# Optimization experiments

Hardware: AMD Instinct MI355X
Metric: run time of the kernel (lower is better)

The kernel has to match this reference:

```python
import jax, jax.numpy as jnp
import numpy as np

N = 1_048_576   # nodes
E = 8_388_608   # edges
G = 32_768      # graphs
D = 9           # node embedding dim (hardcoded emb_dim=9 in source)
H = 2 * D       # GIN MLP hidden
L = 3           # num_layers
ATOM_V, BOND_V = 119, 6
BN_EPS = 1e-5


def setup_inputs() -> dict:
    key = jax.random.key(0)
    ks = jax.random.split(key, 12)
    f = lambda i, shape: jax.random.normal(ks[i], shape, jnp.float32) * 0.1
    return {
        'atom_emb': f(0, (9, ATOM_V, D)),
        'bond_emb': f(1, (L, 3, BOND_V, D)),
        'eps_gin': jnp.zeros((L,), jnp.float32),
        'W1': f(2, (L, D, H)), 'b1': jnp.zeros((L, H)),
        'bn1_g': jnp.ones((L, H)), 'bn1_b': jnp.zeros((L, H)),
        'W2': f(3, (L, H, D)), 'b2': jnp.zeros((L, D)),
        'bno_g': jnp.ones((L, D)), 'bno_b': jnp.zeros((L, D)),
        'vnW1': f(4, (L - 1, D, H)), 'vnb1': jnp.zeros((L - 1, H)),
        'vnbn1_g': jnp.ones((L - 1, H)), 'vnbn1_b': jnp.zeros((L - 1, H)),
        'vnW2': f(5, (L - 1, H, D)), 'vnb2': jnp.zeros((L - 1, D)),
        'vnbn2_g': jnp.ones((L - 1, D)), 'vnbn2_b': jnp.zeros((L - 1, D)),
        'x': jax.random.randint(ks[6], (N, 9), 0, 2),
        'edge_index': jax.random.randint(ks[7], (2, E), 0, N),
        'edge_attr': jax.random.randint(ks[8], (E, 3), 0, 2),
        'batch': jnp.sort(jax.random.randint(ks[9], (N,), 0, G)),
        'num_graphs': G,
    }


def _bn(h, g, b):
    # BatchNorm1d in training mode: batch mean / biased variance
    m = h.mean(axis=0)
    v = h.var(axis=0)
    return (h - m) * jax.lax.rsqrt(v + BN_EPS) * g + b


def reference(atom_emb, bond_emb, eps_gin, W1, b1, bn1_g, bn1_b, W2, b2,
              bno_g, bno_b, vnW1, vnb1, vnbn1_g, vnbn1_b, vnW2, vnb2,
              vnbn2_g, vnbn2_b, x, edge_index, edge_attr, batch, num_graphs):
    n_nodes = x.shape[0]
    src, dst = edge_index[0], edge_index[1]
    # AtomEncoder: sum of per-field embeddings -> [N, D]
    h = atom_emb[jnp.arange(atom_emb.shape[0])[None, :], x].sum(axis=1)
    vn = jnp.zeros((num_graphs, h.shape[1]), h.dtype)  # virtualnode emb init 0
    num_layers = W1.shape[0]
    for l in range(num_layers):
        h_in = h + vn[batch]                              # broadcast VN to nodes
        # BondEncoder for this layer -> [E, D]
        e = bond_emb[l][jnp.arange(3)[None, :], edge_attr].sum(axis=1)
        # GIN message: relu(x_j + e), sum-aggregate at target
        msg = jax.nn.relu(h_in[src] + e)
        aggr = jax.ops.segment_sum(msg, dst, num_segments=n_nodes)
        z = (1.0 + eps_gin[l]) * h_in + aggr
        z = jax.nn.relu(_bn(z @ W1[l] + b1[l], bn1_g[l], bn1_b[l])) @ W2[l] + b2[l]
        z = _bn(z, bno_g[l], bno_b[l])
        if l < num_layers - 1:
            z = jax.nn.relu(z)
        h_new = z + h_in                                   # residual=True
        if l < num_layers - 1:
            vn_tmp = jax.ops.segment_sum(h_in, batch, num_segments=num_graphs) + vn
            t = jax.nn.relu(_bn(vn_tmp @ vnW1[l] + vnb1[l], vnbn1_g[l], vnbn1_b[l]))
            t = jax.nn.relu(_bn(t @ vnW2[l] + vnb2[l], vnbn2_g[l], vnbn2_b[l]))
            vn = vn + t                                    # VN residual
        h = h_new
    pooled = jax.ops.segment_sum(h, batch, num_segments=num_graphs)  # global_add_pool
    return jnp.sum(pooled, axis=0, keepdims=True)          # [1, D]
```

## Files before the change

kernel.cpp:

```cpp
#include <hip/hip_runtime.h>
#include <hip/hip_fp8.h>

#define NN 1048576
#define NE 8388608
#define NG 32768
#define DD 9
#define HH 18
#define BN_EPS 1e-5f

#define NPB 512
#define NB  2048
#define NGRP 64
#define P1B 512
#define P3MAX 5120
#define P3KEYS 2048

#define NSUM1 0
#define NSQ1  18
#define NSUM2 36
#define NSQ2  45
#define OUTS  54
#define VBASE 4096
#define VSUM1 (VBASE+0)
#define VSQ1  (VBASE+18)
#define VSUM2 (VBASE+36)
#define VSQ2  (VBASE+45)
#define STATS_FLOATS 4224

typedef float fv4 __attribute__((ext_vector_type(4)));
typedef unsigned uv4 __attribute__((ext_vector_type(4)));

__device__ __forceinline__ float waveReduce(float v) {
#pragma unroll
  for (int off = 32; off > 0; off >>= 1) v += __shfl_down(v, off, 64);
  return v;
}
__device__ __forceinline__ unsigned f8enc(float f) {
  __hip_fp8_e4m3 v(f);
  return (unsigned)v.__x;
}
__device__ __forceinline__ float f8dec(unsigned b) {
  __hip_fp8_e4m3 v;
  v.__x = (__hip_fp8_storage_t)b;
  return (float)v;
}
__device__ __forceinline__ unsigned bf16r(float x) {
  unsigned u = __float_as_uint(x);
  unsigned r = u + 0x7FFFu + ((u >> 16) & 1u);
  return r >> 16;
}
__device__ __forceinline__ unsigned pk2(float a, float b) {
  return bf16r(a) | (bf16r(b) << 16);
}
__device__ __forceinline__ float lo16(unsigned u) { return __uint_as_float(u << 16); }
__device__ __forceinline__ float hi16(unsigned u) { return __uint_as_float(u & 0xFFFF0000u); }

__device__ __forceinline__ void pack9(uv4* __restrict__ b8, unsigned short* __restrict__ b1,
                                      size_t n, const float* v) {
  uv4 p;
  p.x = pk2(v[0], v[1]); p.y = pk2(v[2], v[3]);
  p.z = pk2(v[4], v[5]); p.w = pk2(v[6], v[7]);
  __builtin_nontemporal_store(p, &b8[n]);
  __builtin_nontemporal_store((unsigned short)bf16r(v[8]), &b1[n]);
}
__device__ __forceinline__ void unpack9(const uv4* __restrict__ b8,
                                        const unsigned short* __restrict__ b1,
                                        size_t n, float* v) {
  uv4 P = __builtin_nontemporal_load(&b8[n]);
  unsigned short s = b1[n];
  v[0] = lo16(P.x); v[1] = hi16(P.x); v[2] = lo16(P.y); v[3] = hi16(P.y);
  v[4] = lo16(P.z); v[5] = hi16(P.z); v[6] = lo16(P.w); v[7] = hi16(P.w);
  v[8] = __uint_as_float((unsigned)s << 16);
}


__global__ void __launch_bounds__(1024)
k_counthist(const int* __restrict__ ei, int* __restrict__ cnt_pad,
            int* __restrict__ blkcnt) {
  __shared__ int hist[NB];
  int tid = threadIdx.x;
  for (int i = tid; i < NB; i += 1024) hist[i] = 0;
  __syncthreads();
  const int CH = NE / P1B;
  int base = blockIdx.x * CH;
  for (int i = tid; i < CH; i += 1024)
    atomicAdd(&hist[ei[NE + base + i] >> 9], 1);
  __syncthreads();
  for (int i = tid; i < NB; i += 1024)
    if (hist[i]) atomicAdd(&cnt_pad[i * 16], hist[i]);
  if (tid < NGRP) {
    int s = 0;
#pragma unroll
    for (int k = 0; k < 32; ++k) s += hist[tid * 32 + k];
    blkcnt[tid * P1B + blockIdx.x] = s;
  }
}

__global__ void k_scan(const int* __restrict__ cnt_pad, int* __restrict__ bucket_base,
                       int* __restrict__ bucket_cursor) {
  __shared__ int tsum[256];
  int tid = threadIdx.x;
  int c[8];
  int run = 0;
#pragma unroll
  for (int k = 0; k < 8; ++k) { c[k] = cnt_pad[(tid * 8 + k) * 16]; run += c[k]; }
  tsum[tid] = run;
  __syncthreads();
  for (int off = 1; off < 256; off <<= 1) {
    int v = (tid >= off) ? tsum[tid - off] : 0;
    __syncthreads();
    tsum[tid] += v;
    __syncthreads();
  }
  int excl = tsum[tid] - run;
#pragma unroll
  for (int k = 0; k < 8; ++k) {
    bucket_base[tid * 8 + k] = excl;
    bucket_cursor[tid * 8 + k] = excl;
    excl += c[k];
  }
  if (tid == 255) bucket_base[NB] = tsum[255];
}

__global__ void k_scanG(int* __restrict__ blkcnt, const int* __restrict__ bucket_base) {
  __shared__ int tsum[256];
  int tid = threadIdx.x;
  int g = blockIdx.x;
  int c0 = blkcnt[g * P1B + 2 * tid], c1 = blkcnt[g * P1B + 2 * tid + 1];
  int run = c0 + c1;
  tsum[tid] = run;
  __syncthreads();
  for (int off = 1; off < 256; off <<= 1) {
    int v = (tid >= off) ? tsum[tid - off] : 0;
    __syncthreads();
    tsum[tid] += v;
    __syncthreads();
  }
  int excl = tsum[tid] - run + bucket_base[g << 5];
  blkcnt[g * P1B + 2 * tid] = excl;
  blkcnt[g * P1B + 2 * tid + 1] = excl + c0;
}

__global__ void __launch_bounds__(1024)
k_p1(const int* __restrict__ ei, const int* __restrict__ ea,
     const int* __restrict__ blkcnt, uint2* __restrict__ coarse) {
  __shared__ int lcnt[NGRP];
  __shared__ int lbase[NGRP];
  int tid = threadIdx.x;
  if (tid < NGRP) { lcnt[tid] = 0; lbase[tid] = blkcnt[tid * P1B + blockIdx.x]; }
  __syncthreads();
  const int CH = NE / P1B;
  int base = blockIdx.x * CH;
  for (int k = 0; k < CH / 1024; ++k) {
    int e = base + k * 1024 + tid;
    int s = ei[e];
    int d = ei[NE + e];
    unsigned at = (unsigned)((ea[(size_t)e * 3 + 0] & 1) |
                             ((ea[(size_t)e * 3 + 1] & 1) << 1) |
                             ((ea[(size_t)e * 3 + 2] & 1) << 2));
    int g = d >> 14;
    int pos = atomicAdd(&lcnt[g], 1);
    coarse[lbase[g] + pos] = make_uint2((unsigned)s | (at << 20), (unsigned)d);
  }
}

#define P2K 48
#define P2SUB 32
__global__ void __launch_bounds__(256)
k_p2(const uint2* __restrict__ coarse, const int* __restrict__ bucket_base,
     int* __restrict__ bucket_cursor, unsigned* __restrict__ binned) {
  __shared__ unsigned stage[32 * P2K];
  __shared__ int scnt[32], gbase[32];
  int tid = threadIdx.x;
  int g = blockIdx.x >> 5;
  int sub = blockIdx.x & 31;
  int s0 = bucket_base[g << 5];
  int s1 = bucket_base[(g + 1) << 5];
  int len = s1 - s0;
  int chunk = (len + P2SUB - 1) >> 5;
  int my0 = s0 + sub * chunk;
  int my1 = min(my0 + chunk, s1);
  if (tid < 32) scnt[tid] = 0;
  __syncthreads();
  for (int b0 = my0; b0 < my1; b0 += 1024) {
#pragma unroll
    for (int k = 0; k < 4; ++k) {
      int i = b0 + k * 256 + tid;
      if (i < my1) {
        uint2 rec = coarse[i];
        unsigned s = rec.x & 0xFFFFFu;
        unsigned at = rec.x >> 20;
        unsigned d = rec.y;
        int bt = (int)((d >> 9) & 31u);
        unsigned o = s | ((d & 511u) << 20) | (at << 29);
        int pos = atomicAdd(&scnt[bt], 1);
        if (pos < P2K) stage[bt * P2K + pos] = o;
        else binned[atomicAdd(&bucket_cursor[(g << 5) | bt], 1)] = o;
      }
    }
    __syncthreads();
    {
      int bt = tid >> 3, j = tid & 7;
      int cnt = min(scnt[bt], P2K);
      if (j == 0) gbase[bt] = cnt ? atomicAdd(&bucket_cursor[(g << 5) | bt], cnt) : 0;
      __syncthreads();
      for (int i = j; i < cnt; i += 8) binned[gbase[bt] + i] = stage[bt * P2K + i];
    }
    __syncthreads();
    if (tid < 32) scnt[tid] = 0;
    __syncthreads();
  }
}

__global__ void __launch_bounds__(256)
k_p3(unsigned* __restrict__ binned, const int* __restrict__ bucket_base,
     int* __restrict__ row_ptr, unsigned* __restrict__ rpo) {
  __shared__ int cnt[P3KEYS];
  __shared__ int tsum[256];
  __shared__ unsigned stage[P3MAX];
  int tid = threadIdx.x;
  int b = blockIdx.x;
  int s0 = bucket_base[b], s1 = bucket_base[b + 1];
  int len = s1 - s0;
  for (int i = tid; i < P3KEYS; i += 256) cnt[i] = 0;
  __syncthreads();
  for (int i = tid; i < len; i += 256) {
    unsigned rec = binned[s0 + i];
    int key = (int)((((rec >> 20) & 511u) << 2) | ((rec & 0xFFFFFu) >> 18));
    atomicAdd(&cnt[key], 1);
  }
  __syncthreads();
  int c[8];
  int run = 0;
#pragma unroll
  for (int k = 0; k < 8; ++k) { c[k] = cnt[tid * 8 + k]; run += c[k]; }
  tsum[tid] = run;
  __syncthreads();
  for (int off = 1; off < 256; off <<= 1) {
    int v = (tid >= off) ? tsum[tid - off] : 0;
    __syncthreads();
    tsum[tid] += v;
    __syncthreads();
  }
  int excl = tsum[tid] - run;
  int sum4 = c[0] + c[1] + c[2] + c[3];
  row_ptr[b * NPB + 2 * tid] = s0 + excl;
  row_ptr[b * NPB + 2 * tid + 1] = s0 + excl + sum4;
  if (b == NB - 1 && tid == 255) row_ptr[NN] = s0 + excl + run;
  {
    unsigned roA = 0, roB = 0;
    int rA = 0, rB = 0;
#pragma unroll
    for (int k = 0; k < 4; ++k) {
      rA += c[k];      roA |= (unsigned)rA << (k * 8);
      rB += c[4 + k];  roB |= (unsigned)rB << (k * 8);
    }
    rpo[(size_t)b * NPB + 2 * tid] = roA;
    rpo[(size_t)b * NPB + 2 * tid + 1] = roB;
  }
  int e = excl;
#pragma unroll
  for (int k = 0; k < 8; ++k) { cnt[tid * 8 + k] = e; e += c[k]; }
  __syncthreads();
  for (int i = tid; i < len; i += 256) {
    unsigned rec = binned[s0 + i];
    int key = (int)((((rec >> 20) & 511u) << 2) | ((rec & 0xFFFFFu) >> 18));
    int pos = atomicAdd(&cnt[key], 1);
    stage[pos] = (rec & 0xFFFFFu) | ((rec >> 29) << 20);
  }
  __syncthreads();
  for (int i = tid; i < len; i += 256) binned[s0 + i] = stage[i];
}


__device__ __forceinline__ void writeMirror(uint2* __restrict__ hmA,
                                            unsigned char* __restrict__ hmB,
                                            size_t n, const float* hv) {
  uint2 q;
  q.x = f8enc(hv[0]) | (f8enc(hv[1]) << 8) | (f8enc(hv[2]) << 16) | (f8enc(hv[3]) << 24);
  q.y = f8enc(hv[4]) | (f8enc(hv[5]) << 8) | (f8enc(hv[6]) << 16) | (f8enc(hv[7]) << 24);
  hmA[n] = q;
  hmB[n] = (unsigned char)f8enc(hv[8]);
}

__global__ void k_atom(const float* __restrict__ atom_emb, const int* __restrict__ x,
                       const int* __restrict__ batch,
                       uv4* __restrict__ hb8, unsigned short* __restrict__ hb1,
                       uint2* __restrict__ hmA, unsigned char* __restrict__ hmB,
                       float* __restrict__ vnsum) {
  int n = blockIdx.x * 256 + threadIdx.x;
  int xi[9];
#pragma unroll
  for (int f = 0; f < 9; ++f) xi[f] = x[(size_t)n * 9 + f];
  float acc[DD] = {0.f,0.f,0.f,0.f,0.f,0.f,0.f,0.f,0.f};
#pragma unroll
  for (int f = 0; f < 9; ++f) {
    const float* row = atom_emb + ((size_t)f * 119 + xi[f]) * DD;
#pragma unroll
    for (int d = 0; d < DD; ++d) acc[d] += row[d];
  }
  pack9(hb8, hb1, (size_t)n, acc);
  writeMirror(hmA, hmB, (size_t)n, acc);
  int g = batch[n];
  int lane = threadIdx.x & 63;
  float s[DD];
#pragma unroll
  for (int d = 0; d < DD; ++d) s[d] = acc[d];
#pragma unroll
  for (int st = 1; st < 64; st <<= 1) {
    int gu = __shfl_up(g, st, 64);
    bool ok = (lane >= st) && (gu == g);
#pragma unroll
    for (int d = 0; d < DD; ++d) {
      float vu = __shfl_up(s[d], st, 64);
      if (ok) s[d] += vu;
    }
  }
  int gn = __shfl_down(g, 1, 64);
  if ((lane == 63) || (gn != g)) {
#pragma unroll
    for (int d = 0; d < DD; ++d) atomicAdd(&vnsum[(size_t)g * DD + d], s[d]);
  }
}

__device__ __forceinline__ void edgeDecodeAcc(unsigned r, uint2 q, unsigned db,
                                              const float* __restrict__ comb,
                                              float* __restrict__ acc) {
  const float* cb = comb + (r >> 20) * DD;
  float hv[DD] = {f8dec(q.x & 255u), f8dec((q.x >> 8) & 255u),
                  f8dec((q.x >> 16) & 255u), f8dec(q.x >> 24),
                  f8dec(q.y & 255u), f8dec((q.y >> 8) & 255u),
                  f8dec((q.y >> 16) & 255u), f8dec(q.y >> 24),
                  f8dec(db)};
#pragma unroll
  for (int d = 0; d < DD; ++d) {
    float m = hv[d] + cb[d];
    m = m > 0.f ? m : 0.f;
    acc[d] += m;
  }
}

__device__ __forceinline__ void accumNode(const unsigned* __restrict__ binned,
                                          int e0, int e1,
                                          const uint2* __restrict__ hmA,
                                          const unsigned char* __restrict__ hmB,
                                          const float* __restrict__ comb,
                                          float* __restrict__ acc) {
  int i = e0;
  for (; i + 4 <= e1; i += 4) {
    unsigned r0 = binned[i], r1 = binned[i + 1], r2 = binned[i + 2], r3 = binned[i + 3];
    uint2 q0 = hmA[r0 & 0xFFFFFu];
    uint2 q1 = hmA[r1 & 0xFFFFFu];
    uint2 q2 = hmA[r2 & 0xFFFFFu];
    uint2 q3 = hmA[r3 & 0xFFFFFu];
    unsigned char d0 = hmB[r0 & 0xFFFFFu];
    unsigned char d1 = hmB[r1 & 0xFFFFFu];
    unsigned char d2 = hmB[r2 & 0xFFFFFu];
    unsigned char d3 = hmB[r3 & 0xFFFFFu];
    edgeDecodeAcc(r0, q0, d0, comb, acc);
    edgeDecodeAcc(r1, q1, d1, comb, acc);
    edgeDecodeAcc(r2, q2, d2, comb, acc);
    edgeDecodeAcc(r3, q3, d3, comb, acc);
  }
  for (; i < e1; ++i) {
    unsigned r = binned[i];
    uint2 q = hmA[r & 0xFFFFFu];
    unsigned char db = hmB[r & 0xFFFFFu];
    edgeDecodeAcc(r, q, db, comb, acc);
  }
}

__global__ void __launch_bounds__(256, 8)
k_edgeA(const uv4* __restrict__ hb8, const unsigned short* __restrict__ hb1,
        const uint2* __restrict__ hmA,
        const unsigned char* __restrict__ hmB, const unsigned* __restrict__ binned,
        const int* __restrict__ row_ptr, const unsigned* __restrict__ rpo,
        const float* __restrict__ bond,
        const float* __restrict__ W1l, const float* __restrict__ b1l,
        const float* __restrict__ epsp, uv4* __restrict__ X8,
        unsigned short* __restrict__ X1, float* __restrict__ stats) {
  __shared__ float comb[8 * DD];
  __shared__ float sW1[DD * HH], sb1[HH], ssum[HH], ssq[HH];
  int tid = threadIdx.x;
  for (int i = tid; i < DD * HH; i += 256) sW1[i] = W1l[i];
  if (tid < 8 * DD) {
    int c = tid / DD, d = tid % DD;
    comb[tid] = bond[(0 * 6 + (c & 1)) * DD + d] +
                bond[(1 * 6 + ((c >> 1) & 1)) * DD + d] +
                bond[(2 * 6 + ((c >> 2) & 1)) * DD + d];
  }
  if (tid < HH) { sb1[tid] = b1l[tid]; ssum[tid] = 0.f; ssq[tid] = 0.f; }
  __syncthreads();

  int b = blockIdx.x;
  int nA = b * NPB + tid;
  int nB = nA + 256;
  int ea0 = row_ptr[nA];
  int eb0 = row_ptr[nB];
  unsigned roA = rpo[nA], roB = rpo[nB];
  float acc0[DD] = {0.f,0.f,0.f,0.f,0.f,0.f,0.f,0.f,0.f};
  float acc1[DD] = {0.f,0.f,0.f,0.f,0.f,0.f,0.f,0.f,0.f};

  int pA = ea0, pB = eb0;
#pragma unroll
  for (int q = 0; q < 4; ++q) {
    int eA = ea0 + (int)((roA >> (q * 8)) & 255u);
    int eB = eb0 + (int)((roB >> (q * 8)) & 255u);
    accumNode(binned, pA, eA, hmA, hmB, comb, acc0);
    accumNode(binned, pB, eB, hmA, hmB, comb, acc1);
    pA = eA;
    pB = eB;
    __syncthreads();
  }

  float eps1 = 1.0f + epsp[0];
  float z0[DD], z1[DD];
  {
    float hi[DD];
    unpack9(hb8, hb1, (size_t)nA, hi);
#pragma unroll
    for (int d = 0; d < DD; ++d) z0[d] = eps1 * hi[d] + acc0[d];
    pack9(X8, X1, (size_t)nA, z0);
  }
  {
    float hi[DD];
    unpack9(hb8, hb1, (size_t)nB, hi);
#pragma unroll
    for (int d = 0; d < DD; ++d) z1[d] = eps1 * hi[d] + acc1[d];
    pack9(X8, X1, (size_t)nB, z1);
  }
  int lane0 = ((tid & 63) == 0);
#pragma unroll
  for (int j = 0; j < HH; ++j) {
    float a0 = sb1[j], a1 = sb1[j];
#pragma unroll
    for (int d = 0; d < DD; ++d) {
      a0 += z0[d] * sW1[d * HH + j];
      a1 += z1[d] * sW1[d * HH + j];
    }
    float rs = waveReduce(a0 + a1);
    float rq = waveReduce(a0 * a0 + a1 * a1);
    if (lane0) { atomicAdd(&ssum[j], rs); atomicAdd(&ssq[j], rq); }
  }
  __syncthreads();
  int copy = (b & 63) * 64;
  if (tid < HH) {
    atomicAdd(&stats[copy + NSUM1 + tid], ssum[tid]);
    atomicAdd(&stats[copy + NSQ1 + tid], ssq[tid]);
  }
}

__global__ void __launch_bounds__(256)
k_partB(uv4* __restrict__ X8, unsigned short* __restrict__ X1,
        const float* __restrict__ W1l, const float* __restrict__ b1l,
        const float* __restrict__ g1, const float* __restrict__ be1,
        const float* __restrict__ W2l, const float* __restrict__ b2l,
        float* __restrict__ stats) {
  __shared__ float sW1[DD * HH], sW2[HH * DD], sb1[HH], sb2[DD];
  __shared__ float sc1[HH], sh1[HH], ssum[DD], ssq[DD];
  int tid = threadIdx.x;
  for (int i = tid; i < DD * HH; i += 256) sW1[i] = W1l[i];
  for (int i = tid; i < HH * DD; i += 256) sW2[i] = W2l[i];
  if (tid < HH) {
    float s = 0.f, q = 0.f;
#pragma unroll
    for (int c = 0; c < 64; ++c) {
      s += stats[c * 64 + NSUM1 + tid];
      q += stats[c * 64 + NSQ1 + tid];
    }
    float mean = s * (1.0f / NN);
    float var = q * (1.0f / NN) - mean * mean;
    float sc = g1[tid] * rsqrtf(var + BN_EPS);
    sc1[tid] = sc;
    sh1[tid] = be1[tid] - mean * sc;
    sb1[tid] = b1l[tid];
  }
  if (tid < DD) { sb2[tid] = b2l[tid]; ssum[tid] = 0.f; ssq[tid] = 0.f; }
  __syncthreads();
  size_t n = (size_t)blockIdx.x * 256 + tid;
  float z[DD];
  unpack9(X8, X1, n, z);
  float t[HH];
#pragma unroll
  for (int j = 0; j < HH; ++j) {
    float a = sb1[j];
#pragma unroll
    for (int d = 0; d < DD; ++d) a += z[d] * sW1[d * HH + j];
    a = a * sc1[j] + sh1[j];
    t[j] = a > 0.f ? a : 0.f;
  }
  float z2[DD];
  int lane0 = ((tid & 63) == 0);
#pragma unroll
  for (int d = 0; d < DD; ++d) {
    float a = sb2[d];
#pragma unroll
    for (int j = 0; j < HH; ++j) a += t[j] * sW2[j * DD + d];
    z2[d] = a;
    float rs = waveReduce(a);
    float rq = waveReduce(a * a);
    if (lane0) { atomicAdd(&ssum[d], rs); atomicAdd(&ssq[d], rq); }
  }
  pack9(X8, X1, n, z2);
  __syncthreads();
  int copy = ((int)blockIdx.x & 63) * 64;
  if (tid < DD) {
    atomicAdd(&stats[copy + NSUM2 + tid], ssum[tid]);
    atomicAdd(&stats[copy + NSQ2 + tid], ssq[tid]);
  }
}

__global__ void __launch_bounds__(256)
k_partC(const uv4* __restrict__ X8, const unsigned short* __restrict__ X1,
        uv4* __restrict__ hb8, unsigned short* __restrict__ hb1,
        uint2* __restrict__ hmA, unsigned char* __restrict__ hmB,
        float* __restrict__ stats, const float* __restrict__ g2,
        const float* __restrict__ be2, const int* __restrict__ batch,
        const float* __restrict__ vn_next, float* __restrict__ vnsum_out,
        int do_relu) {
  __shared__ float sc[DD], sh[DD], ssum[DD];
  int tid = threadIdx.x;
  if (tid < DD) {
    float s = 0.f, q = 0.f;
#pragma unroll
    for (int c = 0; c < 64; ++c) {
      s += stats[c * 64 + NSUM2 + tid];
      q += stats[c * 64 + NSQ2 + tid];
    }
    float mean = s * (1.0f / NN);
    float var = q * (1.0f / NN) - mean * mean;
    float sg = g2[tid] * rsqrtf(var + BN_EPS);
    sc[tid] = sg;
    sh[tid] = be2[tid] - mean * sg;
    ssum[tid] = 0.f;
  }
  __syncthreads();
  size_t n = (size_t)blockIdx.x * 256 + tid;
  float zv[DD];
  unpack9(X8, X1, n, zv);
  float hi[DD];
  unpack9(hb8, hb1, n, hi);
  float hv[DD];
#pragma unroll
  for (int d = 0; d < DD; ++d) {
    float z = zv[d] * sc[d] + sh[d];
    if (do_relu) z = z > 0.f ? z : 0.f;
    hv[d] = z + hi[d];
  }
  if (vn_next != nullptr) {
    int g = batch[n];
#pragma unroll
    for (int d = 0; d < DD; ++d) hv[d] += vn_next[(size_t)g * DD + d];
    pack9(hb8, hb1, n, hv);
    writeMirror(hmA, hmB, n, hv);
    if (vnsum_out != nullptr) {
      int lane = tid & 63;
      float s[DD];
#pragma unroll
      for (int d = 0; d < DD; ++d) s[d] = hv[d];
#pragma unroll
      for (int st = 1; st < 64; st <<= 1) {
        int gu = __shfl_up(g, st, 64);
        bool ok = (lane >= st) && (gu == g);
#pragma unroll
        for (int d = 0; d < DD; ++d) {
          float vu = __shfl_up(s[d], st, 64);
          if (ok) s[d] += vu;
        }
      }
      int gn = __shfl_down(g, 1, 64);
      if ((lane == 63) || (gn != g)) {
#pragma unroll
        for (int d = 0; d < DD; ++d) atomicAdd(&vnsum_out[(size_t)g * DD + d], s[d]);
      }
    }
  } else {
    int lane0 = ((tid & 63) == 0);
#pragma unroll
    for (int d = 0; d < DD; ++d) {
      float r = waveReduce(hv[d]);
      if (lane0) atomicAdd(&ssum[d], r);
    }
    __syncthreads();
    int copy = ((int)blockIdx.x & 63) * 64;
    if (tid < DD) atomicAdd(&stats[copy + OUTS + tid], ssum[tid]);
  }
}

__global__ void k_out(const float* __restrict__ stats, float* __restrict__ out) {
  int tid = threadIdx.x;
  if (tid < DD) {
    float s = 0.f;
#pragma unroll
    for (int c = 0; c < 64; ++c) s += stats[c * 64 + OUTS + tid];
    out[tid] = s;
  }
}


__global__ void k_vnA(const float* __restrict__ vnsum, const float* __restrict__ vn,
                      float* __restrict__ vt1, const float* __restrict__ W1l,
                      const float* __restrict__ b1l, float* __restrict__ stats) {
  __shared__ float sW[DD * HH], sb[HH], ssum[HH], ssq[HH];
  int tid = threadIdx.x;
  for (int i = tid; i < DD * HH; i += 256) sW[i] = W1l[i];
  if (tid < HH) { sb[tid] = b1l[tid]; ssum[tid] = 0.f; ssq[tid] = 0.f; }
  __syncthreads();
  size_t g = (size_t)blockIdx.x * 256 + tid;
  float r[DD];
#pragma unroll
  for (int d = 0; d < DD; ++d) r[d] = vnsum[g * DD + d] + vn[g * DD + d];
  int lane0 = ((tid & 63) == 0);
#pragma unroll
  for (int j = 0; j < HH; ++j) {
    float a = sb[j];
#pragma unroll
    for (int d = 0; d < DD; ++d) a += r[d] * sW[d * HH + j];
    vt1[g * HH + j] = a;
    float rs = waveReduce(a);
    float rq = waveReduce(a * a);
    if (lane0) { atomicAdd(&ssum[j], rs); atomicAdd(&ssq[j], rq); }
  }
  __syncthreads();
  if (tid < HH) {
    atomicAdd(&stats[VSUM1 + tid], ssum[tid]);
    atomicAdd(&stats[VSQ1 + tid], ssq[tid]);
  }
}

__global__ void k_vnB(const float* __restrict__ vt1, float* __restrict__ vt2,
                      const float* __restrict__ W2l, const float* __restrict__ b2l,
                      const float* __restrict__ g1, const float* __restrict__ be1,
                      float* __restrict__ stats) {
  __shared__ float sW2[HH * DD], sb2[DD], sc1[HH], sh1[HH], ssum[DD], ssq[DD];
  int tid = threadIdx.x;
  for (int i = tid; i < HH * DD; i += 256) sW2[i] = W2l[i];
  if (tid < HH) {
    float mean = stats[VSUM1 + tid] * (1.0f / NG);
    float var = stats[VSQ1 + tid] * (1.0f / NG) - mean * mean;
    float sc = g1[tid] * rsqrtf(var + BN_EPS);
    sc1[tid] = sc;
    sh1[tid] = be1[tid] - mean * sc;
  }
  if (tid < DD) { sb2[tid] = b2l[tid]; ssum[tid] = 0.f; ssq[tid] = 0.f; }
  __syncthreads();
  size_t g = (size_t)blockIdx.x * 256 + tid;
  float t[HH];
#pragma unroll
  for (int j = 0; j < HH; ++j) {
    float a = vt1[g * HH + j] * sc1[j] + sh1[j];
    t[j] = a > 0.f ? a : 0.f;
  }
  int lane0 = ((tid & 63) == 0);
#pragma unroll
  for (int d = 0; d < DD; ++d) {
    float a = sb2[d];
#pragma unroll
    for (int j = 0; j < HH; ++j) a += t[j] * sW2[j * DD + d];
    vt2[g * DD + d] = a;
    float rs = waveReduce(a);
    float rq = waveReduce(a * a);
    if (lane0) { atomicAdd(&ssum[d], rs); atomicAdd(&ssq[d], rq); }
  }
  __syncthreads();
  if (tid < DD) {
    atomicAdd(&stats[VSUM2 + tid], ssum[tid]);
    atomicAdd(&stats[VSQ2 + tid], ssq[tid]);
  }
}

__global__ void k_vnC(const float* __restrict__ vt2, float* __restrict__ vn,
                      const float* __restrict__ g2, const float* __restrict__ be2,
                      const float* __restrict__ stats) {
  __shared__ float sc[DD], sh[DD];
  int tid = threadIdx.x;
  if (tid < DD) {
    float mean = stats[VSUM2 + tid] * (1.0f / NG);
    float var = stats[VSQ2 + tid] * (1.0f / NG) - mean * mean;
    float s = g2[tid] * rsqrtf(var + BN_EPS);
    sc[tid] = s;
    sh[tid] = be2[tid] - mean * s;
  }
  __syncthreads();
  size_t g = (size_t)blockIdx.x * 256 + tid;
#pragma unroll
  for (int d = 0; d < DD; ++d) {
    float v = vt2[g * DD + d] * sc[d] + sh[d];
    v = v > 0.f ? v : 0.f;
    vn[g * DD + d] += v;
  }
}

extern "C" void kernel_launch(void* const* d_in, const int* in_sizes, int n_in,
                              void* d_out, int out_size, void* d_ws, size_t ws_size,
                              hipStream_t stream) {
  const float* atom_emb = (const float*)d_in[0];
  const float* bond_emb = (const float*)d_in[1];
  const float* eps_gin  = (const float*)d_in[2];
  const float* W1   = (const float*)d_in[3];
  const float* b1   = (const float*)d_in[4];
  const float* bn1_g = (const float*)d_in[5];
  const float* bn1_b = (const float*)d_in[6];
  const float* W2   = (const float*)d_in[7];
  const float* b2   = (const float*)d_in[8];
  const float* bno_g = (const float*)d_in[9];
  const float* bno_b = (const float*)d_in[10];
  const float* vnW1 = (const float*)d_in[11];
  const float* vnb1 = (const float*)d_in[12];
  const float* vnbn1_g = (const float*)d_in[13];
  const float* vnbn1_b = (const float*)d_in[14];
  const float* vnW2 = (const float*)d_in[15];
  const float* vnb2 = (const float*)d_in[16];
  const float* vnbn2_g = (const float*)d_in[17];
  const float* vnbn2_b = (const float*)d_in[18];
  const int* x          = (const int*)d_in[19];
  const int* edge_index = (const int*)d_in[20];
  const int* edge_attr  = (const int*)d_in[21];
  const int* batch      = (const int*)d_in[22];
  float* out = (float*)d_out;

  char* base = (char*)d_ws;
  uv4* hb8 = (uv4*)base;
  unsigned short* hb1 = (unsigned short*)(hb8 + (size_t)NN);
  uv4* X8 = (uv4*)(hb1 + (size_t)NN);
  unsigned short* X1 = (unsigned short*)(X8 + (size_t)NN);
  uint2* coarse = (uint2*)base;
  int* cnt_pad  = (int*)(coarse + (size_t)NE);
  int* blkcnt   = cnt_pad + (size_t)NB * 16;
  char* pers = (char*)(blkcnt + (size_t)NGRP * P1B);
  uint2* hmA   = (uint2*)pers;
  unsigned char* hmB = (unsigned char*)(hmA + (size_t)NN);
  unsigned* binned = (unsigned*)(hmB + (size_t)NN);
  float* vn    = (float*)(binned + (size_t)NE);
  float* vnsum = vn + (size_t)NG * DD;
  float* vt2   = vnsum;
  float* vt1   = vnsum + (size_t)NG * DD;
  float* stats = vt1 + (size_t)NG * HH;
  int* bucket_base   = (int*)(stats + STATS_FLOATS);
  int* bucket_cursor = bucket_base + NB + 1;
  int* row_ptr       = bucket_cursor + NB;
  unsigned* rpo      = (unsigned*)(row_ptr + NN + 1);

  (void)hipMemsetAsync(cnt_pad, 0, (size_t)NB * 16 * sizeof(int), stream);
  k_counthist<<<P1B, 1024, 0, stream>>>(edge_index, cnt_pad, blkcnt);
  k_scan<<<1, 256, 0, stream>>>(cnt_pad, bucket_base, bucket_cursor);
  k_scanG<<<NGRP, 256, 0, stream>>>(blkcnt, bucket_base);
  k_p1<<<P1B, 1024, 0, stream>>>(edge_index, edge_attr, blkcnt, coarse);
  k_p2<<<NGRP * P2SUB, 256, 0, stream>>>(coarse, bucket_base, bucket_cursor, binned);
  k_p3<<<NB, 256, 0, stream>>>(binned, bucket_base, row_ptr, rpo);

  (void)hipMemsetAsync(vn, 0, (size_t)2 * NG * DD * sizeof(float), stream);
  k_atom<<<NN / 256, 256, 0, stream>>>(atom_emb, x, batch, hb8, hb1, hmA, hmB, vnsum);

  for (int l = 0; l < 3; ++l) {
    int has_vn = (l < 2);
    (void)hipMemsetAsync(stats, 0, STATS_FLOATS * sizeof(float), stream);
    if (has_vn) {
      k_vnA<<<NG / 256, 256, 0, stream>>>(vnsum, vn, vt1, vnW1 + (size_t)l * DD * HH,
                                          vnb1 + (size_t)l * HH, stats);
      k_vnB<<<NG / 256, 256, 0, stream>>>(vt1, vt2, vnW2 + (size_t)l * HH * DD,
                                          vnb2 + (size_t)l * DD,
                                          vnbn1_g + (size_t)l * HH, vnbn1_b + (size_t)l * HH,
                                          stats);
      k_vnC<<<NG / 256, 256, 0, stream>>>(vt2, vn, vnbn2_g + (size_t)l * DD,
                                          vnbn2_b + (size_t)l * DD, stats);
    }
    k_edgeA<<<NB, 256, 0, stream>>>(hb8, hb1, hmA, hmB, binned, row_ptr, rpo,
                                    bond_emb + (size_t)l * 3 * 6 * DD,
                                    W1 + (size_t)l * DD * HH, b1 + (size_t)l * HH,
                                    eps_gin + l, X8, X1, stats);
    k_partB<<<NN / 256, 256, 0, stream>>>(X8, X1, W1 + (size_t)l * DD * HH,
                                          b1 + (size_t)l * HH,
                                          bn1_g + (size_t)l * HH, bn1_b + (size_t)l * HH,
                                          W2 + (size_t)l * HH * DD, b2 + (size_t)l * DD,
                                          stats);
    if (l == 0)
      (void)hipMemsetAsync(vnsum, 0, (size_t)NG * DD * sizeof(float), stream);
    k_partC<<<NN / 256, 256, 0, stream>>>(X8, X1, hb8, hb1, hmA, hmB, stats,
                                          bno_g + (size_t)l * DD, bno_b + (size_t)l * DD,
                                          batch,
                                          has_vn ? vn : nullptr,
                                          (l == 0) ? vnsum : nullptr,
                                          has_vn ? 1 : 0);
  }
  k_out<<<1, 64, 0, stream>>>(stats, out);
}
```

Before: 1.227 ms.

## Fuse virtual-node MLP kernels into one kernel with software grid barriers

Merges the three virtual-node kernels (linear+stats, BN+linear+stats, BN+residual) into one kernel of 128 blocks that keeps intermediates in registers. Two atomic-counter grid barriers replace the kernel boundaries that waited for the BatchNorm statistics. This removes two launches and the global round trips for the vt1/vt2 intermediates. It relies on all 128 blocks being co-resident, which holds on this GPU, and on the barrier counters in the zeroed stats area being reset before every launch.

```diff
diff --git a/kernel.cpp b/kernel.cpp
--- a/kernel.cpp
+++ b/kernel.cpp
@@ -14,6 +14,7 @@
 #define P1B 512
 #define P3MAX 5120
 #define P3KEYS 2048
+#define VNB 128
 
 #define NSUM1 0
 #define NSQ1  18
@@ -25,6 +26,7 @@
 #define VSQ1  (VBASE+18)
 #define VSUM2 (VBASE+36)
 #define VSQ2  (VBASE+45)
+#define BARS  4160
 #define STATS_FLOATS 4224
 
 typedef float fv4 __attribute__((ext_vector_type(4)));
@@ -598,25 +600,50 @@
 }
 
 
-__global__ void k_vnA(const float* __restrict__ vnsum, const float* __restrict__ vn,
-                      float* __restrict__ vt1, const float* __restrict__ W1l,
-                      const float* __restrict__ b1l, float* __restrict__ stats) {
-  __shared__ float sW[DD * HH], sb[HH], ssum[HH], ssq[HH];
-  int tid = threadIdx.x;
-  for (int i = tid; i < DD * HH; i += 256) sW[i] = W1l[i];
-  if (tid < HH) { sb[tid] = b1l[tid]; ssum[tid] = 0.f; ssq[tid] = 0.f; }
+__device__ __forceinline__ void gridBar(int* cnt, int* gen) {
+  __syncthreads();
+  if (threadIdx.x == 0) {
+    __threadfence();
+    int g = atomicAdd(gen, 0);
+    __threadfence();
+    int t = atomicAdd(cnt, 1 | (g >> 31));
+    if (t == VNB - 1) {
+      atomicAdd(gen, 1);
+    } else {
+      while (atomicAdd(gen, 0) == g) __builtin_amdgcn_s_sleep(8);
+    }
+    __threadfence();
+  }
+  __syncthreads();
+}
+
+__global__ void __launch_bounds__(256)
+k_vn(const float* __restrict__ vnsum, float* __restrict__ vn,
+     const float* __restrict__ W1l, const float* __restrict__ b1l,
+     const float* __restrict__ g1, const float* __restrict__ be1,
+     const float* __restrict__ W2l, const float* __restrict__ b2l,
+     const float* __restrict__ g2, const float* __restrict__ be2,
+     float* __restrict__ stats) {
+  __shared__ float sW1[DD * HH], sW2[HH * DD], sb1[HH], sb2[DD];
+  __shared__ float ssum[HH], ssq[HH], sc1[HH], sh1[HH];
+  int tid = threadIdx.x;
+  int* bar = (int*)(stats + BARS);
+  for (int i = tid; i < DD * HH; i += 256) { sW1[i] = W1l[i]; sW2[i] = W2l[i]; }
+  if (tid < HH) { sb1[tid] = b1l[tid]; ssum[tid] = 0.f; ssq[tid] = 0.f; }
+  if (tid < DD) sb2[tid] = b2l[tid];
   __syncthreads();
   size_t g = (size_t)blockIdx.x * 256 + tid;
   float r[DD];
 #pragma unroll
   for (int d = 0; d < DD; ++d) r[d] = vnsum[g * DD + d] + vn[g * DD + d];
   int lane0 = ((tid & 63) == 0);
+  float a1[HH];
 #pragma unroll
   for (int j = 0; j < HH; ++j) {
-    float a = sb[j];
-#pragma unroll
-    for (int d = 0; d < DD; ++d) a += r[d] * sW[d * HH + j];
-    vt1[g * HH + j] = a;
+    float a = sb1[j];
+#pragma unroll
+    for (int d = 0; d < DD; ++d) a += r[d] * sW1[d * HH + j];
+    a1[j] = a;
     float rs = waveReduce(a);
     float rq = waveReduce(a * a);
     if (lane0) { atomicAdd(&ssum[j], rs); atomicAdd(&ssq[j], rq); }
@@ -626,38 +653,31 @@
     atomicAdd(&stats[VSUM1 + tid], ssum[tid]);
     atomicAdd(&stats[VSQ1 + tid], ssq[tid]);
   }
-}
-
-__global__ void k_vnB(const float* __restrict__ vt1, float* __restrict__ vt2,
-                      const float* __restrict__ W2l, const float* __restrict__ b2l,
-                      const float* __restrict__ g1, const float* __restrict__ be1,
-                      float* __restrict__ stats) {
-  __shared__ float sW2[HH * DD], sb2[DD], sc1[HH], sh1[HH], ssum[DD], ssq[DD];
-  int tid = threadIdx.x;
-  for (int i = tid; i < HH * DD; i += 256) sW2[i] = W2l[i];
+  gridBar(&bar[0], &bar[1]);
   if (tid < HH) {
-    float mean = stats[VSUM1 + tid] * (1.0f / NG);
-    float var = stats[VSQ1 + tid] * (1.0f / NG) - mean * mean;
+    float s = atomicAdd(&stats[VSUM1 + tid], 0.0f);
+    float q = atomicAdd(&stats[VSQ1 + tid], 0.0f);
+    float mean = s * (1.0f / NG);
+    float var = q * (1.0f / NG) - mean * mean;
     float sc = g1[tid] * rsqrtf(var + BN_EPS);
     sc1[tid] = sc;
     sh1[tid] = be1[tid] - mean * sc;
   }
-  if (tid < DD) { sb2[tid] = b2l[tid]; ssum[tid] = 0.f; ssq[tid] = 0.f; }
-  __syncthreads();
-  size_t g = (size_t)blockIdx.x * 256 + tid;
+  if (tid < DD) { ssum[tid] = 0.f; ssq[tid] = 0.f; }
+  __syncthreads();
   float t[HH];
 #pragma unroll
   for (int j = 0; j < HH; ++j) {
-    float a = vt1[g * HH + j] * sc1[j] + sh1[j];
+    float a = a1[j] * sc1[j] + sh1[j];
     t[j] = a > 0.f ? a : 0.f;
   }
-  int lane0 = ((tid & 63) == 0);
+  float z2[DD];
 #pragma unroll
   for (int d = 0; d < DD; ++d) {
     float a = sb2[d];
 #pragma unroll
     for (int j = 0; j < HH; ++j) a += t[j] * sW2[j * DD + d];
-    vt2[g * DD + d] = a;
+    z2[d] = a;
     float rs = waveReduce(a);
     float rq = waveReduce(a * a);
     if (lane0) { atomicAdd(&ssum[d], rs); atomicAdd(&ssq[d], rq); }
@@ -667,25 +687,20 @@
     atomicAdd(&stats[VSUM2 + tid], ssum[tid]);
     atomicAdd(&stats[VSQ2 + tid], ssq[tid]);
   }
-}
-
-__global__ void k_vnC(const float* __restrict__ vt2, float* __restrict__ vn,
-                      const float* __restrict__ g2, const float* __restrict__ be2,
-                      const float* __restrict__ stats) {
-  __shared__ float sc[DD], sh[DD];
-  int tid = threadIdx.x;
+  gridBar(&bar[2], &bar[3]);
   if (tid < DD) {
-    float mean = stats[VSUM2 + tid] * (1.0f / NG);
-    float var = stats[VSQ2 + tid] * (1.0f / NG) - mean * mean;
-    float s = g2[tid] * rsqrtf(var + BN_EPS);
-    sc[tid] = s;
-    sh[tid] = be2[tid] - mean * s;
-  }
-  __syncthreads();
-  size_t g = (size_t)blockIdx.x * 256 + tid;
+    float s = atomicAdd(&stats[VSUM2 + tid], 0.0f);
+    float q = atomicAdd(&stats[VSQ2 + tid], 0.0f);
+    float mean = s * (1.0f / NG);
+    float var = q * (1.0f / NG) - mean * mean;
+    float sc = g2[tid] * rsqrtf(var + BN_EPS);
+    sc1[tid] = sc;
+    sh1[tid] = be2[tid] - mean * sc;
+  }
+  __syncthreads();
 #pragma unroll
   for (int d = 0; d < DD; ++d) {
-    float v = vt2[g * DD + d] * sc[d] + sh[d];
+    float v = z2[d] * sc1[d] + sh1[d];
     v = v > 0.f ? v : 0.f;
     vn[g * DD + d] += v;
   }
@@ -733,9 +748,7 @@
   unsigned* binned = (unsigned*)(hmB + (size_t)NN);
   float* vn    = (float*)(binned + (size_t)NE);
   float* vnsum = vn + (size_t)NG * DD;
-  float* vt2   = vnsum;
-  float* vt1   = vnsum + (size_t)NG * DD;
-  float* stats = vt1 + (size_t)NG * HH;
+  float* stats = vnsum + (size_t)NG * DD;
   int* bucket_base   = (int*)(stats + STATS_FLOATS);
   int* bucket_cursor = bucket_base + NB + 1;
   int* row_ptr       = bucket_cursor + NB;
@@ -756,14 +769,12 @@
     int has_vn = (l < 2);
     (void)hipMemsetAsync(stats, 0, STATS_FLOATS * sizeof(float), stream);
     if (has_vn) {
-      k_vnA<<<NG / 256, 256, 0, stream>>>(vnsum, vn, vt1, vnW1 + (size_t)l * DD * HH,
-                                          vnb1 + (size_t)l * HH, stats);
-      k_vnB<<<NG / 256, 256, 0, stream>>>(vt1, vt2, vnW2 + (size_t)l * HH * DD,
-                                          vnb2 + (size_t)l * DD,
-                                          vnbn1_g + (size_t)l * HH, vnbn1_b + (size_t)l * HH,
-                                          stats);
-      k_vnC<<<NG / 256, 256, 0, stream>>>(vt2, vn, vnbn2_g + (size_t)l * DD,
-                                          vnbn2_b + (size_t)l * DD, stats);
+      k_vn<<<VNB, 256, 0, stream>>>(vnsum, vn,
+                                    vnW1 + (size_t)l * DD * HH, vnb1 + (size_t)l * HH,
+                                    vnbn1_g + (size_t)l * HH, vnbn1_b + (size_t)l * HH,
+                                    vnW2 + (size_t)l * HH * DD, vnb2 + (size_t)l * DD,
+                                    vnbn2_g + (size_t)l * DD, vnbn2_b + (size_t)l * DD,
+                                    stats);
     }
     k_edgeA<<<NB, 256, 0, stream>>>(hb8, hb1, hmA, hmB, binned, row_ptr, rpo,
                                     bond_emb + (size_t)l * 3 * 6 * DD,
```

Result: slower. 1.264 ms (+3.0%).
